# Performance work log

Hardware: AMD Instinct MI355X
Metric: run time of the kernel (lower is better)

Reference implementation:

```python
import jax, jax.numpy as jnp
import numpy as np

G, B, T, H = 14, 64, 2048, 6  # nb_gaussians, batch, track_len, nb_hidden_variables
LOG_2PI = float(np.log(2.0 * np.pi))


def _dnn(x, d):
    # tf.math.divide_no_nan, safe under autodiff
    d_safe = jnp.where(d == 0, 1.0, d)
    return jnp.where(d == 0, 0.0, x / d_safe)


def _norm_log_gaussian(t):
    return -0.5 * (LOG_2PI + t ** 2)


def _gaussian_product(c1, c2, n1, n2, b1, b2, k):
    # RNN_gaussian_product: combine gaussians 1,2 so output-3 no longer depends
    # on coef k and output-4 carries it. (Tiny 1e-20/1e-100 TF noise terms are
    # numerically void and omitted.)
    C1 = c1[:, :, k:k + 1]  # [B,T,1]
    C2 = c2[:, :, k:k + 1]
    cc1, cc2 = _dnn(c1, C1), _dnn(c2, C2)
    nn1, nn2 = _dnn(n1, C1), _dnn(n2, C2)
    bb1, bb2 = _dnn(b1, C1[:, :, 0]), _dnn(b2, C2[:, :, 0])
    var1 = 1.0 / C1 ** 2
    var2 = 1.0 / C2 ** 2
    var3 = var1 + var2
    std3 = jnp.sqrt(var3)
    c3 = (cc1 - cc2) / std3
    n3 = (nn1 - nn2) / std3
    b3 = (bb1 - bb2) / std3[:, :, 0]
    var4 = var1 * var2 / var3
    std4 = jnp.sqrt(var4)
    den = var3 * std4
    c4 = (cc1 * var2 + cc2 * var1) / den
    n4 = (nn1 * var2 + nn2 * var1) / den
    b4 = (bb1 * var2[:, :, 0] + bb2 * var1[:, :, 0]) / den[:, :, 0]
    logC = -jnp.log(jnp.abs(C1 * C2 * std4 * std3))[:, :, 0]
    return logC, c3, c4, n3, n4, b3, b4


def _forward(cur, nxt, biases):
    nH = cur.shape[-1]
    cur_l = list(cur)
    nxt_l = list(nxt)
    b_l = list(biases)
    LC = jnp.zeros(cur.shape[1:3], cur.dtype)  # [B,T]
    # Phase 1: integrate out each current hidden variable k.
    for k in range(nH):
        n = len(b_l)
        for i in range(n - 1):
            logC, c3, c4, n3, n4, b3, b4 = _gaussian_product(
                cur_l[i], cur_l[i + 1], nxt_l[i], nxt_l[i + 1], b_l[i], b_l[i + 1], k)
            cur_l[i], cur_l[i + 1] = c3, c4
            nxt_l[i], nxt_l[i + 1] = n3, n4
            b_l[i], b_l[i + 1] = b3, b4
            LC = LC + logC
        # final_RNN_function_phase_1: integrate & drop last dependent gaussian
        LC = LC - jnp.log(jnp.abs(cur_l[n - 1][:, :, k]))
        cur_l.pop(n - 1)
        nxt_l.pop(n - 1)
        b_l.pop(n - 1)
    # Phase 2: roles of current/next swapped; pop dependent gaussian into kept.
    kept_n, kept_b = [], []
    for k in range(nH):
        n = len(b_l)
        for i in range(n - 1):
            logC, n3, n4, c3, c4, b3, b4 = _gaussian_product(
                nxt_l[i], nxt_l[i + 1], cur_l[i], cur_l[i + 1], b_l[i], b_l[i + 1], k)
            nxt_l[i], nxt_l[i + 1] = n3, n4
            cur_l[i], cur_l[i + 1] = c3, c4
            b_l[i], b_l[i + 1] = b3, b4
            LC = LC + logC
        kept_n.append(nxt_l.pop(n - 1))
        kept_b.append(b_l.pop(n - 1))
        cur_l.pop(n - 1)
    # Remaining gaussians are pure constants
    LC = LC + jnp.sum(_norm_log_gaussian(jnp.stack(b_l)), axis=0)
    return jnp.stack(kept_n), jnp.stack(kept_b), LC


def setup_inputs() -> dict:
    key = jax.random.key(0)
    ks = jax.random.split(key, 5)

    def coefs(k1, k2, shape):
        mag = jax.random.uniform(k1, shape, jnp.float32, 0.5, 1.5)
        sgn = jnp.where(jax.random.bernoulli(k2, 0.5, shape), 1.0, -1.0)
        return mag * sgn

    cur = coefs(ks[0], ks[1], (G, B, T, H))
    nxt = coefs(ks[2], ks[3], (G, B, T, H))
    biases = jax.random.normal(ks[4], (G, B, T), jnp.float32)
    return {"current_hidden_var_coefs": cur,
            "next_hidden_var_coefs": nxt,
            "biases": biases}


def reference(current_hidden_var_coefs, next_hidden_var_coefs, biases):
    return _forward(current_hidden_var_coefs, next_hidden_var_coefs, biases)
```

## Files before the change

kernel.cpp:

```cpp
#include <hip/hip_runtime.h>

#define Gc 14
#define Hc 6
#define NPc (64*2048)
#define LOG_2PI 1.8378770664093453f

typedef float v2f __attribute__((ext_vector_type(2)));

__device__ __forceinline__ float frsq(float x){ return __builtin_amdgcn_rsqf(x); }

template<int CTRL>
__device__ __forceinline__ float dppf(float x){
    union { float f; int i; } u; u.f = x;
    u.i = __builtin_amdgcn_update_dpp(0, u.i, CTRL, 0xF, 0xF, true);
    return u.f;
}
template<int OQ>
__device__ __forceinline__ float bcast(float x){
    return (OQ == 0) ? dppf<0xA0>(x) : dppf<0xF5>(x);
}

__device__ __forceinline__ void nt_store_v2f(float* p, v2f v){
    union { v2f f; unsigned long long u; } c; c.f = v;
    __builtin_nontemporal_store(c.u, (unsigned long long*)p);
}

template<int J, int C, int N, int OQ>
__device__ __forceinline__ void sweep(v2f (&st)[Gc][3], float (&bb)[Gc]){
#pragma unroll
    for (int i = 0; i < N - 1; ++i){
        const float C1 = bcast<OQ>(st[i][J][C]);
        const float C2 = bcast<OQ>(st[i + 1][J][C]);
        const float S  = frsq(fmaf(C1, C1, C2 * C2));
        const float s1 = C2 * S, s2 = C1 * S;
        const float a1 = copysignf(s1, C1), a2 = copysignf(s2, C2);
        const v2f A1 = {a1, a1}, A2 = {a2, a2}, S1 = {s1, s1}, S2 = {s2, s2};
#pragma unroll
        for (int j = 0; j < 3; ++j){
            const v2f x = st[i][j], y = st[i + 1][j];
            st[i][j]     = __builtin_elementwise_fma(x, A1, -(y * A2));
            st[i + 1][j] = __builtin_elementwise_fma(x, S2, y * S1);
        }
        {
            const float x = bb[i], y = bb[i + 1];
            bb[i]     = fmaf(x, a1, -(y * a2));
            bb[i + 1] = fmaf(x, s2, y * s1);
        }
    }
}

__global__ void __launch_bounds__(256, 2)
gaussmerge_kernel(const float* __restrict__ cur_in,
                  const float* __restrict__ nxt_in,
                  const float* __restrict__ b_in,
                  float* __restrict__ out)
{
    const int tid = threadIdx.x;
    const int q = tid & 1;
    const int p = blockIdx.x * 128 + (tid >> 1);

    v2f   st[Gc][3];
    float bb[Gc];

    const float* abase = (q ? nxt_in : cur_in) + (size_t)p * Hc;
    const float* bp    = b_in + p;
#pragma unroll
    for (int g = 0; g < Gc; ++g){
        const float* rec = abase + (size_t)g * (NPc * Hc);
        const float4 A = *(const float4*)rec;
        const float2 B = *(const float2*)(rec + 4);
        st[g][0] = (v2f){A.x, A.y};
        st[g][1] = (v2f){A.z, A.w};
        st[g][2] = (v2f){B.x, B.y};
        bb[g] = bp[(size_t)g * NPc];
    }

    float LC = 0.0f;

    sweep<0, 0, 14, 0>(st, bb); LC -= __logf(fabsf(st[13][0][0]));
    sweep<0, 1, 13, 0>(st, bb); LC -= __logf(fabsf(st[12][0][1]));
    sweep<1, 0, 12, 0>(st, bb); LC -= __logf(fabsf(st[11][1][0]));
    sweep<1, 1, 11, 0>(st, bb); LC -= __logf(fabsf(st[10][1][1]));
    sweep<2, 0, 10, 0>(st, bb); LC -= __logf(fabsf(st[ 9][2][0]));
    sweep<2, 1,  9, 0>(st, bb); LC -= __logf(fabsf(st[ 8][2][1]));

    float* outN = out;
    float* outB = out + (size_t)Hc * NPc * Hc;
    float* outL = outB + (size_t)Hc * NPc;

#define PH2(K, J, C, N)                                                         \
    sweep<J, C, N, 1>(st, bb);                                                  \
    {                                                                           \
        constexpr int m = 7 - (K);                                              \
        if (q) {                                                                \
            float* o = outN + (size_t)(K) * (NPc * Hc) + (size_t)p * Hc;        \
            nt_store_v2f(o,     st[m][0]);                                      \
            nt_store_v2f(o + 2, st[m][1]);                                      \
            nt_store_v2f(o + 4, st[m][2]);                                      \
        } else {                                                                \
            __builtin_nontemporal_store(bb[m], outB + (size_t)(K) * NPc + p);   \
        }                                                                       \
    }

    PH2(0, 0, 0, 8)
    PH2(1, 0, 1, 7)
    PH2(2, 1, 0, 6)
    PH2(3, 1, 1, 5)
    PH2(4, 2, 0, 4)
    PH2(5, 2, 1, 3)
#undef PH2

    LC += -0.5f * (LOG_2PI + bb[0] * bb[0]);
    LC += -0.5f * (LOG_2PI + bb[1] * bb[1]);
    if (q == 0) __builtin_nontemporal_store(LC, outL + p);
}

extern "C" void kernel_launch(void* const* d_in, const int* in_sizes, int n_in,
                              void* d_out, int out_size, void* d_ws, size_t ws_size,
                              hipStream_t stream) {
    const float* cur = (const float*)d_in[0];
    const float* nxt = (const float*)d_in[1];
    const float* bia = (const float*)d_in[2];
    float* out = (float*)d_out;

    dim3 grid((NPc * 2) / 256), block(256);
    gaussmerge_kernel<<<grid, block, 0, stream>>>(cur, nxt, bia, out);
}
```

Baseline: 29.81 us.

## Replace sequential Givens rotation sweeps with single Householder reflection per sweep

```diff
diff --git a/kernel.cpp b/kernel.cpp
--- a/kernel.cpp
+++ b/kernel.cpp
@@ -8,6 +8,7 @@
 typedef float v2f __attribute__((ext_vector_type(2)));
 
 __device__ __forceinline__ float frsq(float x){ return __builtin_amdgcn_rsqf(x); }
+__device__ __forceinline__ float frcp(float x){ return __builtin_amdgcn_rcpf(x); }
 
 template<int CTRL>
 __device__ __forceinline__ float dppf(float x){
@@ -25,28 +26,56 @@
     __builtin_nontemporal_store(c.u, (unsigned long long*)p);
 }
 
-template<int J, int C, int N, int OQ>
-__device__ __forceinline__ void sweep(v2f (&st)[Gc][3], float (&bb)[Gc]){
+template<int J, int C, int N, int OQ, bool UPD_LAST>
+__device__ __forceinline__ float hh_sweep(v2f (&st)[Gc][3], float (&bb)[Gc], float* sOut){
+    float q0 = 0.f, q1 = 0.f;
+    v2f d0 = {0.f, 0.f}, d1 = {0.f, 0.f}, d2 = {0.f, 0.f};
+    float db = 0.f;
+    float hl = 0.f;
+#pragma unroll
+    for (int i = 0; i < N; ++i){
+        const float hi = bcast<OQ>(st[i][J][C]);
+        if (i & 1) q1 = fmaf(hi, hi, q1); else q0 = fmaf(hi, hi, q0);
+        const v2f H = {hi, hi};
+        d0 = __builtin_elementwise_fma(H, st[i][0], d0);
+        d1 = __builtin_elementwise_fma(H, st[i][1], d1);
+        d2 = __builtin_elementwise_fma(H, st[i][2], d2);
+        db = fmaf(hi, bb[i], db);
+        if (i == N - 1) hl = hi;
+    }
+    const float q    = q0 + q1;
+    const float rn   = q * frsq(q);
+    const float s    = copysignf(rn, hl);
+    const float vl   = hl + s;
+    const float beta = frcp(fmaf(s, hl, q));
+    {
+        const v2f S2 = {s, s};
+        d0 = __builtin_elementwise_fma(S2, st[N - 1][0], d0);
+        d1 = __builtin_elementwise_fma(S2, st[N - 1][1], d1);
+        d2 = __builtin_elementwise_fma(S2, st[N - 1][2], d2);
+        db = fmaf(s, bb[N - 1], db);
+    }
+    const v2f B2 = {beta, beta};
+    const v2f t0 = d0 * B2, t1 = d1 * B2, t2 = d2 * B2;
+    const float tb = db * beta;
 #pragma unroll
     for (int i = 0; i < N - 1; ++i){
-        const float C1 = bcast<OQ>(st[i][J][C]);
-        const float C2 = bcast<OQ>(st[i + 1][J][C]);
-        const float S  = frsq(fmaf(C1, C1, C2 * C2));
-        const float s1 = C2 * S, s2 = C1 * S;
-        const float a1 = copysignf(s1, C1), a2 = copysignf(s2, C2);
-        const v2f A1 = {a1, a1}, A2 = {a2, a2}, S1 = {s1, s1}, S2 = {s2, s2};
-#pragma unroll
-        for (int j = 0; j < 3; ++j){
-            const v2f x = st[i][j], y = st[i + 1][j];
-            st[i][j]     = __builtin_elementwise_fma(x, A1, -(y * A2));
-            st[i + 1][j] = __builtin_elementwise_fma(x, S2, y * S1);
-        }
-        {
-            const float x = bb[i], y = bb[i + 1];
-            bb[i]     = fmaf(x, a1, -(y * a2));
-            bb[i + 1] = fmaf(x, s2, y * s1);
-        }
+        const float hi = bcast<OQ>(st[i][J][C]);
+        const v2f Hn = {-hi, -hi};
+        st[i][0] = __builtin_elementwise_fma(t0, Hn, st[i][0]);
+        st[i][1] = __builtin_elementwise_fma(t1, Hn, st[i][1]);
+        st[i][2] = __builtin_elementwise_fma(t2, Hn, st[i][2]);
+        bb[i] = fmaf(tb, -hi, bb[i]);
     }
+    if (UPD_LAST){
+        const v2f Vn = {-vl, -vl};
+        st[N - 1][0] = __builtin_elementwise_fma(t0, Vn, st[N - 1][0]);
+        st[N - 1][1] = __builtin_elementwise_fma(t1, Vn, st[N - 1][1]);
+        st[N - 1][2] = __builtin_elementwise_fma(t2, Vn, st[N - 1][2]);
+        bb[N - 1] = fmaf(tb, -vl, bb[N - 1]);
+    }
+    *sOut = s;
+    return rn;
 }
 
 __global__ void __launch_bounds__(256, 2)
@@ -76,29 +105,34 @@
     }
 
     float LC = 0.0f;
+    float sdump;
 
-    sweep<0, 0, 14, 0>(st, bb); LC -= __logf(fabsf(st[13][0][0]));
-    sweep<0, 1, 13, 0>(st, bb); LC -= __logf(fabsf(st[12][0][1]));
-    sweep<1, 0, 12, 0>(st, bb); LC -= __logf(fabsf(st[11][1][0]));
-    sweep<1, 1, 11, 0>(st, bb); LC -= __logf(fabsf(st[10][1][1]));
-    sweep<2, 0, 10, 0>(st, bb); LC -= __logf(fabsf(st[ 9][2][0]));
-    sweep<2, 1,  9, 0>(st, bb); LC -= __logf(fabsf(st[ 8][2][1]));
+    LC -= __logf(hh_sweep<0, 0, 14, 0, false>(st, bb, &sdump));
+    LC -= __logf(hh_sweep<0, 1, 13, 0, false>(st, bb, &sdump));
+    LC -= __logf(hh_sweep<1, 0, 12, 0, false>(st, bb, &sdump));
+    LC -= __logf(hh_sweep<1, 1, 11, 0, false>(st, bb, &sdump));
+    LC -= __logf(hh_sweep<2, 0, 10, 0, false>(st, bb, &sdump));
+    LC -= __logf(hh_sweep<2, 1,  9, 0, false>(st, bb, &sdump));
 
     float* outN = out;
     float* outB = out + (size_t)Hc * NPc * Hc;
     float* outL = outB + (size_t)Hc * NPc;
 
 #define PH2(K, J, C, N)                                                         \
-    sweep<J, C, N, 1>(st, bb);                                                  \
     {                                                                           \
-        constexpr int m = 7 - (K);                                              \
+        float s_;                                                               \
+        (void)hh_sweep<J, C, N, 1, true>(st, bb, &s_);                          \
+        constexpr int m = (N) - 1;                                              \
+        const float flip = -copysignf(1.0f, s_);  \
+        const v2f F = {flip, flip};                                             \
         if (q) {                                                                \
             float* o = outN + (size_t)(K) * (NPc * Hc) + (size_t)p * Hc;        \
-            nt_store_v2f(o,     st[m][0]);                                      \
-            nt_store_v2f(o + 2, st[m][1]);                                      \
-            nt_store_v2f(o + 4, st[m][2]);                                      \
+            nt_store_v2f(o,     st[m][0] * F);                                  \
+            nt_store_v2f(o + 2, st[m][1] * F);                                  \
+            nt_store_v2f(o + 4, st[m][2] * F);                                  \
         } else {                                                                \
-            __builtin_nontemporal_store(bb[m], outB + (size_t)(K) * NPc + p);   \
+            __builtin_nontemporal_store(bb[m] * flip,                           \
+                                        outB + (size_t)(K) * NPc + p);          \
         }                                                                       \
     }
 
```

New measurement: 28.89 us (median of 2 runs). 1.03x faster.
